# Kernel optimization log

Measured on AMD Instinct MI355X. Metric: run time of the kernel, lower is better.

The kernel has to match this reference:

```python
import jax, jax.numpy as jnp
import numpy as np

WAY = 5
SHOT = 5


def setup_inputs() -> dict:
    key = jax.random.key(0)
    k1, k2, k3 = jax.random.split(key, 3)
    x1 = jax.random.normal(k1, (150, 512, 21, 21), dtype=jnp.float32)   # query images
    x2 = jax.random.normal(k2, (25, 512, 21, 21), dtype=jnp.float32)    # support: way*shot
    conv_w = jax.random.normal(k3, (441,), dtype=jnp.float32) * 0.02    # Conv1d(1,1,441) weight, init N(0,0.02)
    conv_b = jnp.zeros((1,), dtype=jnp.float32)                          # Conv1d bias
    return {"x1": x1, "x2": x2, "conv_w": conv_w, "conv_b": conv_b}


def reference(x1, x2, conv_w, conv_b):
    Q, C, H, W = x1.shape
    HW = H * W  # 441

    # ---- cal_covariance_Batch: per-class covariance of centered local descriptors ----
    # (way*shot, C, H, W) -> (way, shot*HW, C)
    f = x2.reshape(x2.shape[0], C, HW).transpose(0, 2, 1).reshape(WAY, SHOT * HW, C)
    f = f - f.mean(axis=1, keepdims=True)
    n = SHOT * HW
    cov = jnp.einsum('wnc,wnd->wcd', f, f) / (n - 1)  # (way, C, C)

    # ---- cal_covasimilarity: diagonal of q @ Cov @ q^T, computed directly ----
    q = x1.reshape(Q, C, HW)
    q = q - q.mean(axis=2, keepdims=True)
    q = q.transpose(0, 2, 1)  # (Q, HW, C)
    qc = jnp.einsum('qic,wcd->qwid', q, cov)          # (Q, way, HW, C)
    sim = jnp.einsum('qwid,qid->qwi', qc, q)          # diag of quadratic form, (Q, way, HW)

    # ---- conv1d_layer: LeakyReLU(0.2) -> Dropout (identity in eval) -> Conv1d(1,1,441,stride=441) ----
    act = jnp.where(sim >= 0, sim, 0.2 * sim)         # (Q, way, HW)
    scores = jnp.einsum('qwk,k->qw', act, conv_w) + conv_b[0]  # (Q, way)
    return scores
```

## Files before the change

kernel.cpp:

```cpp
#include <hip/hip_runtime.h>
#include <hip/hip_bf16.h>

#define QN 150
#define CN 512
#define HWN 441
#define WAYN 5
#define SHOTN 5
#define NSAMP 2205
#define MROWS (QN * HWN)
#define MT128 517
#define MPAD2 66304
#define KP 2208
#define KPB (KP * 2)

typedef unsigned short u16;
typedef unsigned int u32;
typedef __attribute__((ext_vector_type(8))) short short8;
typedef __attribute__((ext_vector_type(4))) float f32x4;

__device__ __forceinline__ u16 f2b(float f) {
    return __builtin_bit_cast(u16, __float2bfloat16(f));
}
__device__ __forceinline__ float b2f(u16 h) {
    u32 u = ((u32)h) << 16;
    return __builtin_bit_cast(float, u);
}

__device__ __forceinline__ void gload16(const void* g, void* l) {
    __builtin_amdgcn_global_load_lds(
        (const __attribute__((address_space(1))) unsigned int*)g,
        (__attribute__((address_space(3))) unsigned int*)l, 16, 0, 0);
}

__device__ __forceinline__ void pair_decode(int p, int& lo, int& hi) {
    hi = (p >= 6) ? 3 : (p >= 3 ? 2 : (p >= 1 ? 1 : 0));
    int tri = (hi == 3) ? 6 : (hi == 2 ? 3 : (hi == 1 ? 1 : 0));
    lo = p - tri;
}

__global__ void wx2c_kernel(const float* __restrict__ x2, u16* __restrict__ x2c) {
    int b = blockIdx.x;
    int w = b >> 9, c = b & 511;
    int lane = threadIdx.x;
    float s = 0.f;
    #pragma unroll
    for (int sh = 0; sh < SHOTN; ++sh) {
        const float* p = x2 + ((size_t)((w * SHOTN + sh) * CN + c)) * HWN;
        for (int i = lane; i < HWN; i += 64) s += p[i];
    }
    #pragma unroll
    for (int off = 32; off > 0; off >>= 1) s += __shfl_down(s, off);
    float m = __shfl(s, 0) * (1.0f / NSAMP);

    u16* dst = x2c + ((size_t)(w * CN + c)) * KP;
    #pragma unroll
    for (int sh = 0; sh < SHOTN; ++sh) {
        const float* p = x2 + ((size_t)((w * SHOTN + sh) * CN + c)) * HWN;
        for (int i = lane; i < HWN; i += 64) dst[sh * HWN + i] = f2b(p[i] - m);
    }
    if (lane < (KP - NSAMP)) dst[NSAMP + lane] = 0;
}

__global__ __launch_bounds__(256, 2) void covmfma_kernel(const u16* __restrict__ x2c,
                                                         float* __restrict__ covf) {
    __shared__ __align__(16) u16 As[2][128 * 32];
    __shared__ __align__(16) u16 Bs[2][128 * 32];
    int z  = blockIdx.z;
    int w  = z / 6, ksp = z - w * 6;
    int kchunks = (ksp < 3) ? 12 : 11;
    int kcoff   = (ksp < 3) ? ksp * 12 : 36 + (ksp - 3) * 11;
    int dblk, cblk;
    pair_decode(blockIdx.x, dblk, cblk);
    int c0 = cblk * 128;
    int d0 = dblk * 128;
    int t = threadIdx.x;
    int lane = t & 63, wid = t >> 6;
    int wr = wid >> 1, wc = wid & 1;
    int rl = lane & 15, g4 = lane >> 4;
    int swz = ((rl >> 1) & 3) << 4;
    int s0 = wid * 2048 + lane * 16;

    const char* gX = (const char*)(x2c + (size_t)w * CN * KP) + kcoff * 64;

    f32x4 acc[4][4];
    #pragma unroll
    for (int mi = 0; mi < 4; ++mi)
        #pragma unroll
        for (int ni = 0; ni < 4; ++ni)
            acc[mi][ni] = (f32x4){0.f, 0.f, 0.f, 0.f};

    int buf = 0;
    #pragma unroll
    for (int j = 0; j < 2; ++j) {
        int s = s0 + j * 1024;
        int row = s >> 6, kbs = (s & 63) ^ (((row >> 1) & 3) << 4);
        gload16(gX + (size_t)(c0 + row) * KPB + kbs, (char*)&As[0][0] + wid * 2048 + j * 1024);
        gload16(gX + (size_t)(d0 + row) * KPB + kbs, (char*)&Bs[0][0] + wid * 2048 + j * 1024);
    }
    __syncthreads();

    for (int ks = 0; ks < kchunks; ++ks) {
        if (ks < kchunks - 1) {
            int koff = (ks + 1) * 64;
            #pragma unroll
            for (int j = 0; j < 2; ++j) {
                int s = s0 + j * 1024;
                int row = s >> 6, kbs = (s & 63) ^ (((row >> 1) & 3) << 4);
                gload16(gX + (size_t)(c0 + row) * KPB + koff + kbs,
                        (char*)&As[buf ^ 1][0] + wid * 2048 + j * 1024);
                gload16(gX + (size_t)(d0 + row) * KPB + koff + kbs,
                        (char*)&Bs[buf ^ 1][0] + wid * 2048 + j * 1024);
            }
        }
        const char* Ab = (const char*)&As[buf][0];
        const char* Bb = (const char*)&Bs[buf][0];
        int kread = (g4 * 16) ^ swz;
        short8 a[4], b[4];
        #pragma unroll
        for (int mi = 0; mi < 4; ++mi)
            a[mi] = *(const short8*)(Ab + (wr * 64 + mi * 16 + rl) * 64 + kread);
        #pragma unroll
        for (int ni = 0; ni < 4; ++ni)
            b[ni] = *(const short8*)(Bb + (wc * 64 + ni * 16 + rl) * 64 + kread);
        #pragma unroll
        for (int mi = 0; mi < 4; ++mi)
            #pragma unroll
            for (int ni = 0; ni < 4; ++ni)
                acc[mi][ni] = __builtin_amdgcn_mfma_f32_16x16x32_bf16(
                    a[mi], b[ni], acc[mi][ni], 0, 0, 0);
        __syncthreads();
        buf ^= 1;
    }

    const float inv = 1.0f / (NSAMP - 1);
    #pragma unroll
    for (int mi = 0; mi < 4; ++mi)
        #pragma unroll
        for (int r = 0; r < 4; ++r) {
            int c = c0 + wr * 64 + mi * 16 + g4 * 4 + r;
            #pragma unroll
            for (int ni = 0; ni < 4; ++ni) {
                int d = d0 + wc * 64 + ni * 16 + rl;
                atomicAdd(&covf[((size_t)w * CN + c) * CN + d], acc[mi][ni][r] * inv);
            }
        }
}

__global__ void cov2b_kernel(const float* __restrict__ covf, u16* __restrict__ covb) {
    int i = blockIdx.x * 256 + threadIdx.x;
    int w = i >> 18;
    int cd = i & ((1 << 18) - 1);
    int c = cd >> 9, d = cd & 511;
    int cb = c >> 7, db = d >> 7;
    size_t src;
    if (cb >= db) src = ((size_t)w << 18) + ((size_t)c << 9) + d;
    else          src = ((size_t)w << 18) + ((size_t)d << 9) + c;
    float v = covf[src];
    if (c >= 256 && d < 256) v *= 2.f;
    covb[i] = f2b(v);
}

__global__ __launch_bounds__(256) void qtrans_kernel(const float* __restrict__ x1,
                                                     u16* __restrict__ Abf) {
    __shared__ u16 S[512][72];
    __shared__ float qm[64];
    int c0 = blockIdx.x * 64;
    int q  = blockIdx.y;
    int t = threadIdx.x;
    int lane = t & 63, cq = t >> 6;

    for (int cc = cq; cc < 64; cc += 4) {
        int c = c0 + cc;
        const float* p = x1 + ((size_t)q * CN + c) * HWN;
        float s = 0.f;
        for (int ic = 0; ic < 8; ++ic) {
            int i = ic * 64 + lane;
            float v = (i < HWN) ? p[i] : 0.f;
            s += v;
            S[i][cc] = f2b(v);
        }
        #pragma unroll
        for (int off = 32; off > 0; off >>= 1) s += __shfl_down(s, off);
        if (lane == 0) qm[cc] = s * (1.0f / HWN);
    }
    __syncthreads();

    int coct = t & 7;
    for (int p = 0; p < 16; ++p) {
        int il = p * 32 + (t >> 3);
        if (il >= HWN) continue;
        short8 v = *(const short8*)(&S[il][coct * 8]);
        short8 o;
        #pragma unroll
        for (int j = 0; j < 8; ++j) {
            float f = b2f((u16)v[j]) - qm[coct * 8 + j];
            o[j] = (short)f2b(f);
        }
        *(short8*)(Abf + ((size_t)(q * HWN + il)) * CN + c0 + coct * 8) = o;
    }
}

__global__ void init2_kernel(float* __restrict__ simws, float* __restrict__ covf,
                             u32* __restrict__ AbfPad32) {
    int tid = blockIdx.x * blockDim.x + threadIdx.x;
    int stride = gridDim.x * blockDim.x;
    int nsim = WAYN * MPAD2;
    for (int i = tid; i < nsim; i += stride) simws[i] = 0.f;
    int ncov = WAYN * CN * CN;
    for (int i = tid; i < ncov; i += stride) covf[i] = 0.f;
    int npadw = (MPAD2 - MROWS) * CN / 2;
    for (int i = tid; i < npadw; i += stride) AbfPad32[i] = 0;
}

__global__ __launch_bounds__(256, 4) void gemm128v_kernel(const u16* __restrict__ Abf,
                                                          const u16* __restrict__ covb,
                                                          float* __restrict__ simws) {
    __shared__ __align__(16) u16 As[2][128 * 32];
    __shared__ __align__(16) u16 Bs[2][128 * 32];
    __shared__ float simpart[128 * 3];

    int x = blockIdx.x & 7;
    int l = blockIdx.x >> 3;
    int g = l / 20;
    int m = x * 65 + g;
    if (m >= MT128) return;
    int inner = l - g * 20;
    int w  = inner % 5;
    int dsl = inner / 5;
    int n0 = dsl * 128;
    int NCH = (dsl < 2) ? 8 : 16;
    int r0 = m * 128;

    int t = threadIdx.x;
    int lane = t & 63, wid = t >> 6;
    int wr = wid >> 1, wc = wid & 1;
    int rl = lane & 15, g4 = lane >> 4;
    int swz = ((rl >> 1) & 3) << 4;
    int kread = (g4 * 16) ^ swz;

    const char* gA = (const char*)(Abf + (size_t)r0 * CN);
    const char* gB = (const char*)(covb + ((size_t)w * CN + n0) * CN);

    f32x4 acc[4][4];
    #pragma unroll
    for (int mi = 0; mi < 4; ++mi)
        #pragma unroll
        for (int ni = 0; ni < 4; ++ni)
            acc[mi][ni] = (f32x4){0.f, 0.f, 0.f, 0.f};

    auto stage_chunk = [&](int kc) {
        int slot = kc & 1;
        int kbyte = kc * 64;
        #pragma unroll
        for (int j = 0; j < 2; ++j) {
            int off = j * 4096 + t * 16;
            int row = off >> 6;
            int kbs = (off & 63) ^ (((row >> 1) & 3) << 4);
            gload16(gA + (size_t)row * 1024 + kbyte + kbs, (char*)&As[slot][0] + off);
            gload16(gB + (size_t)row * 1024 + kbyte + kbs, (char*)&Bs[slot][0] + off);
        }
    };

    auto do_chunk = [&](int c) {
        const char* Ab = (const char*)&As[c & 1][0];
        const char* Bb = (const char*)&Bs[c & 1][0];
        short8 a[4], b[4];
        #pragma unroll
        for (int ni = 0; ni < 4; ++ni) {
            b[ni] = *(const short8*)(Bb + (wc * 64 + ni * 16 + rl) * 64 + kread);
            a[ni] = *(const short8*)(Ab + (wr * 64 + ni * 16 + rl) * 64 + kread);
        }
        __builtin_amdgcn_s_setprio(1);
        #pragma unroll
        for (int mi = 0; mi < 4; ++mi)
            #pragma unroll
            for (int ni = 0; ni < 4; ++ni)
                acc[mi][ni] = __builtin_amdgcn_mfma_f32_16x16x32_bf16(
                    a[mi], b[ni], acc[mi][ni], 0, 0, 0);
        __builtin_amdgcn_s_setprio(0);
    };

    stage_chunk(0);

    #pragma unroll 1
    for (int c = 0; c < NCH; ++c) {
        asm volatile("s_waitcnt vmcnt(0)" ::: "memory");
        __builtin_amdgcn_s_barrier();
        asm volatile("" ::: "memory");
        if (c + 1 < NCH) stage_chunk(c + 1);
        do_chunk(c);
    }

    __syncthreads();
    #pragma unroll
    for (int mi = 0; mi < 4; ++mi) {
        #pragma unroll
        for (int r = 0; r < 4; ++r) {
            int Rl = wr * 64 + mi * 16 + g4 * 4 + r;
            size_t Rg = (size_t)r0 + Rl;
            float s = 0.f;
            #pragma unroll
            for (int ni = 0; ni < 4; ++ni) {
                int d = n0 + wc * 64 + ni * 16 + rl;
                s += acc[mi][ni][r] * b2f(Abf[Rg * CN + d]);
            }
            s += __shfl_xor(s, 1);
            s += __shfl_xor(s, 2);
            s += __shfl_xor(s, 4);
            s += __shfl_xor(s, 8);
            if (rl == 0) simpart[Rl * 3 + wc] = s;
        }
    }
    __syncthreads();
    if (t < 128) {
        float v = simpart[t * 3 + 0] + simpart[t * 3 + 1];
        atomicAdd(&simws[(size_t)w * MPAD2 + r0 + t], v);
    }
}

__global__ void finish_kernel(const float* __restrict__ simws,
                              const float* __restrict__ conv_w,
                              const float* __restrict__ conv_b,
                              float* __restrict__ scores) {
    int q = blockIdx.x, w = blockIdx.y;
    int t = threadIdx.x;
    const float* sp = simws + (size_t)w * MPAD2 + q * HWN;
    float s = 0.f;
    for (int i = t; i < HWN; i += 128) {
        float v = sp[i];
        float a = (v >= 0.f) ? v : 0.2f * v;
        s += a * conv_w[i];
    }
    __shared__ float red[2];
    #pragma unroll
    for (int off = 32; off > 0; off >>= 1) s += __shfl_down(s, off);
    if ((t & 63) == 0) red[t >> 6] = s;
    __syncthreads();
    if (t == 0) scores[q * WAYN + w] = red[0] + red[1] + conv_b[0];
}

extern "C" void kernel_launch(void* const* d_in, const int* in_sizes, int n_in,
                              void* d_out, int out_size, void* d_ws, size_t ws_size,
                              hipStream_t stream) {
    const float* x1     = (const float*)d_in[0];
    const float* x2     = (const float*)d_in[1];
    const float* conv_w = (const float*)d_in[2];
    const float* conv_b = (const float*)d_in[3];
    float* scores = (float*)d_out;

    char* ws = (char*)d_ws;
    u16* covb    = (u16*)ws;
    float* simws = (float*)(ws + 2631680);
    float* covf  = (float*)(ws + 3957760);
    u16* x2c     = (u16*)(ws + 9200640);
    u16* Abf     = (u16*)(ws + 9200640);

    wx2c_kernel<<<WAYN * CN, 64, 0, stream>>>(x2, x2c);
    init2_kernel<<<256, 256, 0, stream>>>(simws, covf, (u32*)(Abf + (size_t)MROWS * CN));
    covmfma_kernel<<<dim3(10, 1, WAYN * 6), 256, 0, stream>>>(x2c, covf);
    cov2b_kernel<<<WAYN * CN * CN / 256, 256, 0, stream>>>(covf, covb);
    qtrans_kernel<<<dim3(8, QN), 256, 0, stream>>>(x1, Abf);
    gemm128v_kernel<<<8 * 65 * 20, 256, 0, stream>>>(Abf, covb, simws);
    finish_kernel<<<dim3(QN, WAYN), 128, 0, stream>>>(simws, conv_w, conv_b, scores);
}
```

Measured before the change: 286.8 us.

## Merge prep kernels so covariance GEMM overlaps query transpose

Merges the support-centering and workspace zeroing into one launch, then merges the covariance MFMA GEMM with the query centering/transpose into a second launch using block-index partitioning. To allow this, the query bf16 buffer now lives at its own workspace offset and no longer aliases x2c. The aim is fewer launches and letting the small covariance GEMM run alongside the bandwidth-bound transpose. The main GEMM's launch bound also drops from 4 to 3 blocks per CU. The merged kernel shares a larger shared-memory allocation across both roles, which may lower occupancy for the transpose blocks.

```diff
diff --git a/kernel.cpp b/kernel.cpp
--- a/kernel.cpp
+++ b/kernel.cpp
@@ -38,112 +38,173 @@
     lo = p - tri;
 }
 
-__global__ void wx2c_kernel(const float* __restrict__ x2, u16* __restrict__ x2c) {
-    int b = blockIdx.x;
-    int w = b >> 9, c = b & 511;
-    int lane = threadIdx.x;
-    float s = 0.f;
-    #pragma unroll
-    for (int sh = 0; sh < SHOTN; ++sh) {
-        const float* p = x2 + ((size_t)((w * SHOTN + sh) * CN + c)) * HWN;
-        for (int i = lane; i < HWN; i += 64) s += p[i];
-    }
-    #pragma unroll
-    for (int off = 32; off > 0; off >>= 1) s += __shfl_down(s, off);
-    float m = __shfl(s, 0) * (1.0f / NSAMP);
-
-    u16* dst = x2c + ((size_t)(w * CN + c)) * KP;
-    #pragma unroll
-    for (int sh = 0; sh < SHOTN; ++sh) {
-        const float* p = x2 + ((size_t)((w * SHOTN + sh) * CN + c)) * HWN;
-        for (int i = lane; i < HWN; i += 64) dst[sh * HWN + i] = f2b(p[i] - m);
-    }
-    if (lane < (KP - NSAMP)) dst[NSAMP + lane] = 0;
-}
-
-__global__ __launch_bounds__(256, 2) void covmfma_kernel(const u16* __restrict__ x2c,
-                                                         float* __restrict__ covf) {
-    __shared__ __align__(16) u16 As[2][128 * 32];
-    __shared__ __align__(16) u16 Bs[2][128 * 32];
-    int z  = blockIdx.z;
-    int w  = z / 6, ksp = z - w * 6;
-    int kchunks = (ksp < 3) ? 12 : 11;
-    int kcoff   = (ksp < 3) ? ksp * 12 : 36 + (ksp - 3) * 11;
-    int dblk, cblk;
-    pair_decode(blockIdx.x, dblk, cblk);
-    int c0 = cblk * 128;
-    int d0 = dblk * 128;
+__global__ __launch_bounds__(256) void prep1_kernel(const float* __restrict__ x2,
+                                                    u16* __restrict__ x2c,
+                                                    float* __restrict__ simws,
+                                                    float* __restrict__ covf,
+                                                    u32* __restrict__ AbfPad32) {
     int t = threadIdx.x;
-    int lane = t & 63, wid = t >> 6;
-    int wr = wid >> 1, wc = wid & 1;
-    int rl = lane & 15, g4 = lane >> 4;
-    int swz = ((rl >> 1) & 3) << 4;
-    int s0 = wid * 2048 + lane * 16;
-
-    const char* gX = (const char*)(x2c + (size_t)w * CN * KP) + kcoff * 64;
-
-    f32x4 acc[4][4];
-    #pragma unroll
-    for (int mi = 0; mi < 4; ++mi)
-        #pragma unroll
-        for (int ni = 0; ni < 4; ++ni)
-            acc[mi][ni] = (f32x4){0.f, 0.f, 0.f, 0.f};
-
-    int buf = 0;
-    #pragma unroll
-    for (int j = 0; j < 2; ++j) {
-        int s = s0 + j * 1024;
-        int row = s >> 6, kbs = (s & 63) ^ (((row >> 1) & 3) << 4);
-        gload16(gX + (size_t)(c0 + row) * KPB + kbs, (char*)&As[0][0] + wid * 2048 + j * 1024);
-        gload16(gX + (size_t)(d0 + row) * KPB + kbs, (char*)&Bs[0][0] + wid * 2048 + j * 1024);
-    }
-    __syncthreads();
-
-    for (int ks = 0; ks < kchunks; ++ks) {
-        if (ks < kchunks - 1) {
-            int koff = (ks + 1) * 64;
-            #pragma unroll
-            for (int j = 0; j < 2; ++j) {
-                int s = s0 + j * 1024;
-                int row = s >> 6, kbs = (s & 63) ^ (((row >> 1) & 3) << 4);
-                gload16(gX + (size_t)(c0 + row) * KPB + koff + kbs,
-                        (char*)&As[buf ^ 1][0] + wid * 2048 + j * 1024);
-                gload16(gX + (size_t)(d0 + row) * KPB + koff + kbs,
-                        (char*)&Bs[buf ^ 1][0] + wid * 2048 + j * 1024);
-            }
-        }
-        const char* Ab = (const char*)&As[buf][0];
-        const char* Bb = (const char*)&Bs[buf][0];
-        int kread = (g4 * 16) ^ swz;
-        short8 a[4], b[4];
+    if (blockIdx.x < 640) {
+        int lane = t & 63, sub = t >> 6;
+        int b = blockIdx.x * 4 + sub;
+        int w = b >> 9, c = b & 511;
+        float s = 0.f;
+        #pragma unroll
+        for (int sh = 0; sh < SHOTN; ++sh) {
+            const float* p = x2 + ((size_t)((w * SHOTN + sh) * CN + c)) * HWN;
+            for (int i = lane; i < HWN; i += 64) s += p[i];
+        }
+        #pragma unroll
+        for (int off = 32; off > 0; off >>= 1) s += __shfl_down(s, off);
+        float m = __shfl(s, 0) * (1.0f / NSAMP);
+
+        u16* dst = x2c + ((size_t)(w * CN + c)) * KP;
+        #pragma unroll
+        for (int sh = 0; sh < SHOTN; ++sh) {
+            const float* p = x2 + ((size_t)((w * SHOTN + sh) * CN + c)) * HWN;
+            for (int i = lane; i < HWN; i += 64) dst[sh * HWN + i] = f2b(p[i] - m);
+        }
+        if (lane < (KP - NSAMP)) dst[NSAMP + lane] = 0;
+    } else {
+        int tid = (blockIdx.x - 640) * 256 + t;
+        int stride = 256 * 256;
+        int nsim = WAYN * MPAD2;
+        for (int i = tid; i < nsim; i += stride) simws[i] = 0.f;
+        int ncov = WAYN * CN * CN;
+        for (int i = tid; i < ncov; i += stride) covf[i] = 0.f;
+        int npadw = (MPAD2 - MROWS) * CN / 2;
+        for (int i = tid; i < npadw; i += stride) AbfPad32[i] = 0;
+    }
+}
+
+__global__ __launch_bounds__(256, 2) void prep2_kernel(const u16* __restrict__ x2c,
+                                                       float* __restrict__ covf,
+                                                       const float* __restrict__ x1,
+                                                       u16* __restrict__ Abf) {
+    __shared__ __align__(16) char smem[73984];
+    int t = threadIdx.x;
+
+    if (blockIdx.x < 300) {
+        u16* As0 = (u16*)smem;
+        u16* Bs0 = (u16*)(smem + 16384);
+        int bid = blockIdx.x;
+        int z = bid / 10;
+        int pr = bid - z * 10;
+        int w  = z / 6, ksp = z - w * 6;
+        int kchunks = (ksp < 3) ? 12 : 11;
+        int kcoff   = (ksp < 3) ? ksp * 12 : 36 + (ksp - 3) * 11;
+        int dblk, cblk;
+        pair_decode(pr, dblk, cblk);
+        int c0 = cblk * 128;
+        int d0 = dblk * 128;
+        int lane = t & 63, wid = t >> 6;
+        int wr = wid >> 1, wc = wid & 1;
+        int rl = lane & 15, g4 = lane >> 4;
+        int swz = ((rl >> 1) & 3) << 4;
+        int s0 = wid * 2048 + lane * 16;
+
+        const char* gX = (const char*)(x2c + (size_t)w * CN * KP) + kcoff * 64;
+
+        f32x4 acc[4][4];
         #pragma unroll
         for (int mi = 0; mi < 4; ++mi)
-            a[mi] = *(const short8*)(Ab + (wr * 64 + mi * 16 + rl) * 64 + kread);
-        #pragma unroll
-        for (int ni = 0; ni < 4; ++ni)
-            b[ni] = *(const short8*)(Bb + (wc * 64 + ni * 16 + rl) * 64 + kread);
+            #pragma unroll
+            for (int ni = 0; ni < 4; ++ni)
+                acc[mi][ni] = (f32x4){0.f, 0.f, 0.f, 0.f};
+
+        int buf = 0;
+        #pragma unroll
+        for (int j = 0; j < 2; ++j) {
+            int s = s0 + j * 1024;
+            int row = s >> 6, kbs = (s & 63) ^ (((row >> 1) & 3) << 4);
+            gload16(gX + (size_t)(c0 + row) * KPB + kbs, (char*)As0 + wid * 2048 + j * 1024);
+            gload16(gX + (size_t)(d0 + row) * KPB + kbs, (char*)Bs0 + wid * 2048 + j * 1024);
+        }
+        __syncthreads();
+
+        for (int ks = 0; ks < kchunks; ++ks) {
+            if (ks < kchunks - 1) {
+                int koff = (ks + 1) * 64;
+                #pragma unroll
+                for (int j = 0; j < 2; ++j) {
+                    int s = s0 + j * 1024;
+                    int row = s >> 6, kbs = (s & 63) ^ (((row >> 1) & 3) << 4);
+                    gload16(gX + (size_t)(c0 + row) * KPB + koff + kbs,
+                            (char*)As0 + (buf ^ 1) * 8192 + wid * 2048 + j * 1024);
+                    gload16(gX + (size_t)(d0 + row) * KPB + koff + kbs,
+                            (char*)Bs0 + (buf ^ 1) * 8192 + wid * 2048 + j * 1024);
+                }
+            }
+            const char* Ab = (const char*)As0 + buf * 8192;
+            const char* Bb = (const char*)Bs0 + buf * 8192;
+            int kread = (g4 * 16) ^ swz;
+            short8 a[4], b[4];
+            #pragma unroll
+            for (int mi = 0; mi < 4; ++mi)
+                a[mi] = *(const short8*)(Ab + (wr * 64 + mi * 16 + rl) * 64 + kread);
+            #pragma unroll
+            for (int ni = 0; ni < 4; ++ni)
+                b[ni] = *(const short8*)(Bb + (wc * 64 + ni * 16 + rl) * 64 + kread);
+            #pragma unroll
+            for (int mi = 0; mi < 4; ++mi)
+                #pragma unroll
+                for (int ni = 0; ni < 4; ++ni)
+                    acc[mi][ni] = __builtin_amdgcn_mfma_f32_16x16x32_bf16(
+                        a[mi], b[ni], acc[mi][ni], 0, 0, 0);
+            __syncthreads();
+            buf ^= 1;
+        }
+
+        const float inv = 1.0f / (NSAMP - 1);
         #pragma unroll
         for (int mi = 0; mi < 4; ++mi)
             #pragma unroll
-            for (int ni = 0; ni < 4; ++ni)
-                acc[mi][ni] = __builtin_amdgcn_mfma_f32_16x16x32_bf16(
-                    a[mi], b[ni], acc[mi][ni], 0, 0, 0);
+            for (int r = 0; r < 4; ++r) {
+                int c = c0 + wr * 64 + mi * 16 + g4 * 4 + r;
+                #pragma unroll
+                for (int ni = 0; ni < 4; ++ni) {
+                    int d = d0 + wc * 64 + ni * 16 + rl;
+                    atomicAdd(&covf[((size_t)w * CN + c) * CN + d], acc[mi][ni][r] * inv);
+                }
+            }
+    } else {
+        u16 (*S)[72] = (u16(*)[72])smem;
+        float* qm = (float*)(smem + 73728);
+        int qb = blockIdx.x - 300;
+        int c0 = (qb & 7) * 64;
+        int q  = qb >> 3;
+        int lane = t & 63, cq = t >> 6;
+
+        for (int cc = cq; cc < 64; cc += 4) {
+            int c = c0 + cc;
+            const float* p = x1 + ((size_t)q * CN + c) * HWN;
+            float s = 0.f;
+            for (int ic = 0; ic < 8; ++ic) {
+                int i = ic * 64 + lane;
+                float v = (i < HWN) ? p[i] : 0.f;
+                s += v;
+                S[i][cc] = f2b(v);
+            }
+            #pragma unroll
+            for (int off = 32; off > 0; off >>= 1) s += __shfl_down(s, off);
+            if (lane == 0) qm[cc] = s * (1.0f / HWN);
+        }
         __syncthreads();
-        buf ^= 1;
-    }
-
-    const float inv = 1.0f / (NSAMP - 1);
-    #pragma unroll
-    for (int mi = 0; mi < 4; ++mi)
-        #pragma unroll
-        for (int r = 0; r < 4; ++r) {
-            int c = c0 + wr * 64 + mi * 16 + g4 * 4 + r;
-            #pragma unroll
-            for (int ni = 0; ni < 4; ++ni) {
-                int d = d0 + wc * 64 + ni * 16 + rl;
-                atomicAdd(&covf[((size_t)w * CN + c) * CN + d], acc[mi][ni][r] * inv);
-            }
-        }
+
+        int coct = t & 7;
+        for (int p = 0; p < 16; ++p) {
+            int il = p * 32 + (t >> 3);
+            if (il >= HWN) continue;
+            short8 v = *(const short8*)(&S[il][coct * 8]);
+            short8 o;
+            #pragma unroll
+            for (int j = 0; j < 8; ++j) {
+                float f = b2f((u16)v[j]) - qm[coct * 8 + j];
+                o[j] = (short)f2b(f);
+            }
+            *(short8*)(Abf + ((size_t)(q * HWN + il)) * CN + c0 + coct * 8) = o;
+        }
+    }
 }
 
 __global__ void cov2b_kernel(const float* __restrict__ covf, u16* __restrict__ covb) {
@@ -160,59 +221,7 @@
     covb[i] = f2b(v);
 }
 
-__global__ __launch_bounds__(256) void qtrans_kernel(const float* __restrict__ x1,
-                                                     u16* __restrict__ Abf) {
-    __shared__ u16 S[512][72];
-    __shared__ float qm[64];
-    int c0 = blockIdx.x * 64;
-    int q  = blockIdx.y;
-    int t = threadIdx.x;
-    int lane = t & 63, cq = t >> 6;
-
-    for (int cc = cq; cc < 64; cc += 4) {
-        int c = c0 + cc;
-        const float* p = x1 + ((size_t)q * CN + c) * HWN;
-        float s = 0.f;
-        for (int ic = 0; ic < 8; ++ic) {
-            int i = ic * 64 + lane;
-            float v = (i < HWN) ? p[i] : 0.f;
-            s += v;
-            S[i][cc] = f2b(v);
-        }
-        #pragma unroll
-        for (int off = 32; off > 0; off >>= 1) s += __shfl_down(s, off);
-        if (lane == 0) qm[cc] = s * (1.0f / HWN);
-    }
-    __syncthreads();
-
-    int coct = t & 7;
-    for (int p = 0; p < 16; ++p) {
-        int il = p * 32 + (t >> 3);
-        if (il >= HWN) continue;
-        short8 v = *(const short8*)(&S[il][coct * 8]);
-        short8 o;
-        #pragma unroll
-        for (int j = 0; j < 8; ++j) {
-            float f = b2f((u16)v[j]) - qm[coct * 8 + j];
-            o[j] = (short)f2b(f);
-        }
-        *(short8*)(Abf + ((size_t)(q * HWN + il)) * CN + c0 + coct * 8) = o;
-    }
-}
-
-__global__ void init2_kernel(float* __restrict__ simws, float* __restrict__ covf,
-                             u32* __restrict__ AbfPad32) {
-    int tid = blockIdx.x * blockDim.x + threadIdx.x;
-    int stride = gridDim.x * blockDim.x;
-    int nsim = WAYN * MPAD2;
-    for (int i = tid; i < nsim; i += stride) simws[i] = 0.f;
-    int ncov = WAYN * CN * CN;
-    for (int i = tid; i < ncov; i += stride) covf[i] = 0.f;
-    int npadw = (MPAD2 - MROWS) * CN / 2;
-    for (int i = tid; i < npadw; i += stride) AbfPad32[i] = 0;
-}
-
-__global__ __launch_bounds__(256, 4) void gemm128v_kernel(const u16* __restrict__ Abf,
+__global__ __launch_bounds__(256, 3) void gemm128v_kernel(const u16* __restrict__ Abf,
                                                           const u16* __restrict__ covb,
                                                           float* __restrict__ simws) {
     __shared__ __align__(16) u16 As[2][128 * 32];
@@ -353,13 +362,11 @@
     float* simws = (float*)(ws + 2631680);
     float* covf  = (float*)(ws + 3957760);
     u16* x2c     = (u16*)(ws + 9200640);
-    u16* Abf     = (u16*)(ws + 9200640);
-
-    wx2c_kernel<<<WAYN * CN, 64, 0, stream>>>(x2, x2c);
-    init2_kernel<<<256, 256, 0, stream>>>(simws, covf, (u32*)(Abf + (size_t)MROWS * CN));
-    covmfma_kernel<<<dim3(10, 1, WAYN * 6), 256, 0, stream>>>(x2c, covf);
+    u16* Abf     = (u16*)(ws + 20505600);
+
+    prep1_kernel<<<896, 256, 0, stream>>>(x2, x2c, simws, covf, (u32*)(Abf + (size_t)MROWS * CN));
+    prep2_kernel<<<1500, 256, 0, stream>>>(x2c, covf, x1, Abf);
     cov2b_kernel<<<WAYN * CN * CN / 256, 256, 0, stream>>>(covf, covb);
-    qtrans_kernel<<<dim3(8, QN), 256, 0, stream>>>(x1, Abf);
     gemm128v_kernel<<<8 * 65 * 20, 256, 0, stream>>>(Abf, covb, simws);
     finish_kernel<<<dim3(QN, WAYN), 128, 0, stream>>>(simws, conv_w, conv_b, scores);
 }
```

New measurement: 271.1 us. 5.5% less time.
